# Kernel tuning notes

Measured on AMD Instinct MI355X. Metric: run time of the kernel, lower is better.

The kernel has to match this reference:

```python
import jax, jax.numpy as jnp
from jax import lax
import numpy as np

T, B, IN, H = 512, 256, 128, 512
TAU_MIN, TAU_MAX, DT = 0.2, 2.0, 0.1


def setup_inputs() -> dict:
    key = jax.random.key(0)
    ks = jax.random.split(key, 7)
    s_zh = 1.0 / np.sqrt(IN + H)  # torch Linear default init scale (fan_in)
    s_h = 1.0 / np.sqrt(H)
    return {
        "x_seq": jax.random.normal(ks[0], (T, B, IN), dtype=jnp.float32),
        "Wc": jax.random.uniform(ks[1], (IN + H, H), jnp.float32, -s_zh, s_zh),
        "bc": jax.random.uniform(ks[2], (H,), jnp.float32, -s_zh, s_zh),
        "Wt": jax.random.uniform(ks[3], (IN + H, H), jnp.float32, -s_zh, s_zh),
        "bt": jax.random.uniform(ks[4], (H,), jnp.float32, -s_zh, s_zh),
        "Wo": jax.random.uniform(ks[5], (H, 1), jnp.float32, -s_h, s_h),
        "bo": jax.random.uniform(ks[6], (1,), jnp.float32, -s_h, s_h),
    }


def reference(x_seq, Wc, bc, Wt, bt, Wo, bo):
    # Liquid time-constant RNN: sequential scan over T timesteps.
    def step(h, x_t):
        z = jnp.concatenate([x_t, h], axis=-1)           # [B, IN+H]
        candidate = jnp.tanh(z @ Wc + bc)                # [B, H]
        tau = TAU_MIN + jax.nn.sigmoid(z @ Wt + bt) * (TAU_MAX - TAU_MIN)
        h_next = h + DT * (-h + candidate) / tau         # ODE Euler update
        y_t = h_next @ Wo + bo                           # [B, 1]
        return h_next, (y_t, tau)

    h0 = jnp.zeros((x_seq.shape[1], Wc.shape[1]), dtype=x_seq.dtype)
    _, (y_seq, tau_seq) = lax.scan(step, h0, x_seq)
    return y_seq, tau_seq
```

## Files before the change

kernel.cpp:

```cpp
#include <hip/hip_runtime.h>
#include <stdint.h>

#define T_STEPS 512
#define BATCH   256
#define INP     128
#define HID     512
#define BGN     16
#define CGN     8
#define RB      16
#define CB      64
#define ZP      648

typedef float f32x4 __attribute__((ext_vector_type(4)));
typedef short s16x8 __attribute__((ext_vector_type(8)));
typedef unsigned short u16;
typedef unsigned int   u32;
typedef unsigned long long u64;

__device__ __forceinline__ u32 f2bf(float f) {
  union { float f; u32 u; } v; v.f = f;
  return (v.u + 0x7fffu + ((v.u >> 16) & 1u)) >> 16;
}


__global__ __launch_bounds__(256, 1)
void liquid_persistent(const float* __restrict__ x_seq,
                       const float* __restrict__ Wc, const float* __restrict__ bc,
                       const float* __restrict__ Wt, const float* __restrict__ bt,
                       const float* __restrict__ Wo, const float* __restrict__ bo,
                       float* __restrict__ y_out, float* __restrict__ tau_out,
                       u16* __restrict__ hb, int* __restrict__ flags)
{
  const int tid  = threadIdx.x;
  const int l    = tid & 63;
  const int w    = tid >> 6;
  const int quad = l >> 4;
  const int ln   = l & 15;
  const int bg   = blockIdx.x & (BGN - 1);
  const int cg   = blockIdx.x >> 4;
  const int R0   = bg * RB;
  const int C0   = cg * CB;
  const int cn   = C0 + w * 16 + ln;

  __shared__ u16 zS[RB][ZP];

  s16x8 wfC[20], wfT[20];
#pragma unroll
  for (int kt = 0; kt < 20; ++kt) {
#pragma unroll
    for (int j = 0; j < 8; ++j) {
      int k = kt * 32 + quad * 8 + j;
      wfC[kt][j] = (short)f2bf(Wc[k * HID + cn]);
      wfT[kt][j] = (short)f2bf(Wt[k * HID + cn]);
    }
  }

  const float bcv = bc[cn], btv = bt[cn], wov = Wo[cn];
  const float boadd = (cg == 0 && w == 0) ? bo[0] : 0.0f;
  float hm[4] = {0.f, 0.f, 0.f, 0.f};

  const int xrow = tid >> 4;
  const int xseg = tid & 15;
  int* myflags = flags + bg * (CGN * 16);

  {
    const float* xp = x_seq + ((size_t)0 * BATCH + R0 + xrow) * INP + xseg * 8;
    float4 a = *(const float4*)xp;
    float4 b = *(const float4*)(xp + 4);
    u64 w0 = (u64)f2bf(a.x) | ((u64)f2bf(a.y) << 16) |
             ((u64)f2bf(a.z) << 32) | ((u64)f2bf(a.w) << 48);
    u64 w1 = (u64)f2bf(b.x) | ((u64)f2bf(b.y) << 16) |
             ((u64)f2bf(b.z) << 32) | ((u64)f2bf(b.w) << 48);
    *(u64*)&zS[xrow][xseg * 8]     = w0;
    *(u64*)&zS[xrow][xseg * 8 + 4] = w1;
  }
  __syncthreads();

  for (int t = 0; t < T_STEPS; ++t) {
    const int p = t & 1;

    f32x4 aC0 = {0.f,0.f,0.f,0.f}, aC1 = {0.f,0.f,0.f,0.f};
    f32x4 aT0 = {0.f,0.f,0.f,0.f}, aT1 = {0.f,0.f,0.f,0.f};
    const u16* zb = &zS[ln][quad * 8];
    {
      s16x8 a0 = *(const s16x8*)(zb);
      s16x8 a1 = *(const s16x8*)(zb + 32);
      s16x8 a2 = *(const s16x8*)(zb + 64);
      s16x8 a3 = *(const s16x8*)(zb + 96);
      aC0 = __builtin_amdgcn_mfma_f32_16x16x32_bf16(a0, wfC[0], aC0, 0,0,0);
      aT0 = __builtin_amdgcn_mfma_f32_16x16x32_bf16(a0, wfT[0], aT0, 0,0,0);
      aC1 = __builtin_amdgcn_mfma_f32_16x16x32_bf16(a1, wfC[1], aC1, 0,0,0);
      aT1 = __builtin_amdgcn_mfma_f32_16x16x32_bf16(a1, wfT[1], aT1, 0,0,0);
      aC0 = __builtin_amdgcn_mfma_f32_16x16x32_bf16(a2, wfC[2], aC0, 0,0,0);
      aT0 = __builtin_amdgcn_mfma_f32_16x16x32_bf16(a2, wfT[2], aT0, 0,0,0);
      aC1 = __builtin_amdgcn_mfma_f32_16x16x32_bf16(a3, wfC[3], aC1, 0,0,0);
      aT1 = __builtin_amdgcn_mfma_f32_16x16x32_bf16(a3, wfT[3], aT1, 0,0,0);
    }

    const int tn = (t + 1 < T_STEPS) ? t + 1 : t;
    const float* xp = x_seq + ((size_t)tn * BATCH + R0 + xrow) * INP + xseg * 8;
    float4 xr0 = *(const float4*)xp;
    float4 xr1 = *(const float4*)(xp + 4);

    if (t > 0 && tid < CGN) {
      while (__hip_atomic_load(&myflags[tid * 16], __ATOMIC_RELAXED,
                               __HIP_MEMORY_SCOPE_AGENT) < t) { }
    }
    __syncthreads();

    {
      u64 hv[8];
      u64* hrow = (u64*)hb + ((size_t)p * BATCH + R0 + xrow) * (HID / 4);
#pragma unroll
      for (int i = 0; i < 8; ++i)
        hv[i] = __hip_atomic_load(&hrow[i * 16 + xseg], __ATOMIC_RELAXED,
                                  __HIP_MEMORY_SCOPE_AGENT);
#pragma unroll
      for (int i = 0; i < 8; ++i)
        *(u64*)&zS[xrow][INP + (i * 16 + xseg) * 4] = hv[i];
    }
    __syncthreads();

#pragma unroll
    for (int kt = 4; kt < 20; kt += 2) {
      s16x8 a0 = *(const s16x8*)(zb + kt * 32);
      s16x8 a1 = *(const s16x8*)(zb + kt * 32 + 32);
      aC0 = __builtin_amdgcn_mfma_f32_16x16x32_bf16(a0, wfC[kt],   aC0, 0,0,0);
      aT0 = __builtin_amdgcn_mfma_f32_16x16x32_bf16(a0, wfT[kt],   aT0, 0,0,0);
      aC1 = __builtin_amdgcn_mfma_f32_16x16x32_bf16(a1, wfC[kt+1], aC1, 0,0,0);
      aT1 = __builtin_amdgcn_mfma_f32_16x16x32_bf16(a1, wfT[kt+1], aT1, 0,0,0);
    }
    aC0 += aC1;
    aT0 += aT1;

    {
      u64 w0 = (u64)f2bf(xr0.x) | ((u64)f2bf(xr0.y) << 16) |
               ((u64)f2bf(xr0.z) << 32) | ((u64)f2bf(xr0.w) << 48);
      u64 w1 = (u64)f2bf(xr1.x) | ((u64)f2bf(xr1.y) << 16) |
               ((u64)f2bf(xr1.z) << 32) | ((u64)f2bf(xr1.w) << 48);
      *(u64*)&zS[xrow][xseg * 8]     = w0;
      *(u64*)&zS[xrow][xseg * 8 + 4] = w1;
    }

    float tauv[4];
#pragma unroll
    for (int r = 0; r < 4; ++r) {
      float pc = aC0[r] + bcv;
      float pt = aT0[r] + btv;
      pc = fminf(fmaxf(pc, -20.f), 20.f);
      float e  = __expf(2.f * pc);
      float cand = (e - 1.f) / (e + 1.f);
      float tau  = 0.2f + 1.8f / (1.f + __expf(-pt));
      hm[r] += 0.1f * (cand - hm[r]) / tau;
      tauv[r] = tau;
    }
#pragma unroll
    for (int r = 0; r < 4; ++r) {
      tau_out[((size_t)t * BATCH + R0 + quad * 4 + r) * HID + cn] = tauv[r];
    }

#pragma unroll
    for (int r = 0; r < 4; ++r) {
      u32 bits = f2bf(hm[r]);
      u32 ob   = (u32)__shfl_xor((int)bits, 1);
      if (!(ln & 1)) {
        u32 pk = bits | (ob << 16);
        u32* hp = (u32*)hb +
            (((size_t)(p ^ 1) * BATCH + R0 + quad * 4 + r) * HID + cn) / 2;
        __hip_atomic_store(hp, pk, __ATOMIC_RELAXED, __HIP_MEMORY_SCOPE_AGENT);
      }
    }

#pragma unroll
    for (int r = 0; r < 4; ++r) {
      float py = hm[r] * wov;
      py += __shfl_down(py, 8, 16);
      py += __shfl_down(py, 4, 16);
      py += __shfl_down(py, 2, 16);
      py += __shfl_down(py, 1, 16);
      if (ln == 0)
        atomicAdd(&y_out[t * BATCH + R0 + quad * 4 + r], py + boadd);
    }

    __syncthreads();
    if (tid == 0) {
      __hip_atomic_store(&myflags[cg * 16], t + 1, __ATOMIC_RELAXED,
                         __HIP_MEMORY_SCOPE_AGENT);
    }
  }
}

extern "C" void kernel_launch(void* const* d_in, const int* in_sizes, int n_in,
                              void* d_out, int out_size, void* d_ws, size_t ws_size,
                              hipStream_t stream) {
  (void)in_sizes; (void)n_in; (void)out_size; (void)ws_size;
  const float* x_seq = (const float*)d_in[0];
  const float* Wc    = (const float*)d_in[1];
  const float* bc    = (const float*)d_in[2];
  const float* Wt    = (const float*)d_in[3];
  const float* bt    = (const float*)d_in[4];
  const float* Wo    = (const float*)d_in[5];
  const float* bo    = (const float*)d_in[6];

  float* y_out   = (float*)d_out;
  float* tau_out = (float*)d_out + (size_t)T_STEPS * BATCH;

  const size_t HB_BYTES   = (size_t)2 * BATCH * HID * sizeof(u16);
  const size_t FLAG_BYTES = (size_t)BGN * CGN * 16 * sizeof(int);
  u16* hb    = (u16*)d_ws;
  int* flags = (int*)((char*)d_ws + HB_BYTES);

  hipMemsetAsync(d_out, 0, (size_t)T_STEPS * BATCH * sizeof(float), stream);
  hipMemsetAsync(d_ws, 0, HB_BYTES + FLAG_BYTES, stream);

  liquid_persistent<<<dim3(BGN * CGN), dim3(256), 0, stream>>>(
      x_seq, Wc, bc, Wt, bt, Wo, bo, y_out, tau_out, hb, flags);
}
```

Baseline: 2.033 ms.

## Replace flag barrier with sentinel-tagged 4-slot hidden-state ring buffer

Removes the per-step flag spin plus block barrier and instead encodes readiness in the data itself: a 4-deep ring of bf16 hidden-state buffers is poisoned with 0xFFFF sentinels, and each block polls only the seven peer column chunks until valid values appear. The block's own chunk is written straight from registers into shared memory, and the hidden-state publish is packed into 64-bit stores. This is meant to cut the latency of the inter-block handoff on the recurrent critical path, at the cost of relying on NaN-pattern sentinels never matching real bf16 data and extra store traffic for re-poisoning slots.

```diff
diff --git a/kernel.cpp b/kernel.cpp
--- a/kernel.cpp
+++ b/kernel.cpp
@@ -29,7 +29,7 @@
                        const float* __restrict__ Wt, const float* __restrict__ bt,
                        const float* __restrict__ Wo, const float* __restrict__ bo,
                        float* __restrict__ y_out, float* __restrict__ tau_out,
-                       u16* __restrict__ hb, int* __restrict__ flags)
+                       u16* __restrict__ hb)
 {
   const int tid  = threadIdx.x;
   const int l    = tid & 63;
@@ -61,7 +61,14 @@
 
   const int xrow = tid >> 4;
   const int xseg = tid & 15;
-  int* myflags = flags + bg * (CGN * 16);
+
+  int ii[7];
+#pragma unroll
+  for (int jx = 0; jx < 7; ++jx) ii[jx] = jx + (jx >= cg ? 1 : 0);
+
+  const size_t rowq = HID / 4;
+  u64* hbase = (u64*)(void*)hb;
+  const size_t myrow = (size_t)(R0 + xrow) * rowq;
 
   {
     const float* xp = x_seq + ((size_t)0 * BATCH + R0 + xrow) * INP + xseg * 8;
@@ -77,7 +84,15 @@
   __syncthreads();
 
   for (int t = 0; t < T_STEPS; ++t) {
-    const int p = t & 1;
+    const u64* rbase = hbase + (size_t)(t & 3) * BATCH * rowq + myrow + xseg;
+
+    u64 tmp[7];
+    if (t > 0) {
+#pragma unroll
+      for (int jx = 0; jx < 7; ++jx)
+        tmp[jx] = __hip_atomic_load(rbase + ii[jx] * 16, __ATOMIC_RELAXED,
+                                    __HIP_MEMORY_SCOPE_AGENT);
+    }
 
     f32x4 aC0 = {0.f,0.f,0.f,0.f}, aC1 = {0.f,0.f,0.f,0.f};
     f32x4 aT0 = {0.f,0.f,0.f,0.f}, aT1 = {0.f,0.f,0.f,0.f};
@@ -97,28 +112,58 @@
       aT1 = __builtin_amdgcn_mfma_f32_16x16x32_bf16(a3, wfT[3], aT1, 0,0,0);
     }
 
+    u64 hv[7];
+    if (t == 0) {
+#pragma unroll
+      for (int jx = 0; jx < 7; ++jx) hv[jx] = 0;
+    } else {
+      bool need[7];
+      int pending = 0;
+#pragma unroll
+      for (int jx = 0; jx < 7; ++jx) {
+        u64 v = tmp[jx];
+        bool ok = ((u32)v != 0xFFFFFFFFu) && ((u32)(v >> 32) != 0xFFFFFFFFu);
+        hv[jx] = v;
+        need[jx] = !ok;
+        pending += ok ? 0 : 1;
+      }
+      while (pending) {
+#pragma unroll
+        for (int jx = 0; jx < 7; ++jx)
+          if (need[jx])
+            tmp[jx] = __hip_atomic_load(rbase + ii[jx] * 16, __ATOMIC_RELAXED,
+                                        __HIP_MEMORY_SCOPE_AGENT);
+#pragma unroll
+        for (int jx = 0; jx < 7; ++jx)
+          if (need[jx]) {
+            u64 v = tmp[jx];
+            if (((u32)v != 0xFFFFFFFFu) && ((u32)(v >> 32) != 0xFFFFFFFFu)) {
+              hv[jx] = v;
+              need[jx] = false;
+              --pending;
+            }
+          }
+      }
+    }
+
+    {
+      u64* pp = hbase + (size_t)((t + 2) & 3) * BATCH * rowq + myrow
+              + (C0 / 4 + xseg);
+      __hip_atomic_store(pp, ~0ull, __ATOMIC_RELAXED, __HIP_MEMORY_SCOPE_AGENT);
+    }
+
     const int tn = (t + 1 < T_STEPS) ? t + 1 : t;
     const float* xp = x_seq + ((size_t)tn * BATCH + R0 + xrow) * INP + xseg * 8;
     float4 xr0 = *(const float4*)xp;
     float4 xr1 = *(const float4*)(xp + 4);
 
-    if (t > 0 && tid < CGN) {
-      while (__hip_atomic_load(&myflags[tid * 16], __ATOMIC_RELAXED,
-                               __HIP_MEMORY_SCOPE_AGENT) < t) { }
-    }
-    __syncthreads();
-
-    {
-      u64 hv[8];
-      u64* hrow = (u64*)hb + ((size_t)p * BATCH + R0 + xrow) * (HID / 4);
-#pragma unroll
-      for (int i = 0; i < 8; ++i)
-        hv[i] = __hip_atomic_load(&hrow[i * 16 + xseg], __ATOMIC_RELAXED,
-                                  __HIP_MEMORY_SCOPE_AGENT);
-#pragma unroll
-      for (int i = 0; i < 8; ++i)
-        *(u64*)&zS[xrow][INP + (i * 16 + xseg) * 4] = hv[i];
-    }
+#pragma unroll
+    for (int jx = 0; jx < 7; ++jx)
+      *(u64*)&zS[xrow][INP + (ii[jx] * 16 + xseg) * 4] = hv[jx];
+#pragma unroll
+    for (int r = 0; r < 4; ++r)
+      zS[quad * 4 + r][INP + cn] = (u16)f2bf(hm[r]);
+
     __syncthreads();
 
 #pragma unroll
@@ -154,23 +199,28 @@
       hm[r] += 0.1f * (cand - hm[r]) / tau;
       tauv[r] = tau;
     }
-#pragma unroll
-    for (int r = 0; r < 4; ++r) {
-      tau_out[((size_t)t * BATCH + R0 + quad * 4 + r) * HID + cn] = tauv[r];
-    }
+
+    asm volatile("s_waitcnt vmcnt(0)" ::: "memory");
 
 #pragma unroll
     for (int r = 0; r < 4; ++r) {
       u32 bits = f2bf(hm[r]);
-      u32 ob   = (u32)__shfl_xor((int)bits, 1);
-      if (!(ln & 1)) {
-        u32 pk = bits | (ob << 16);
-        u32* hp = (u32*)hb +
-            (((size_t)(p ^ 1) * BATCH + R0 + quad * 4 + r) * HID + cn) / 2;
-        __hip_atomic_store(hp, pk, __ATOMIC_RELAXED, __HIP_MEMORY_SCOPE_AGENT);
+      u32 b0   = bits | ((u32)__shfl_xor((int)bits, 1) << 16);
+      u64 q    = (u64)b0 | ((u64)(u32)__shfl_xor((int)b0, 2) << 32);
+      if (!(ln & 3)) {
+        u64* hp = hbase + (size_t)((t + 1) & 3) * BATCH * rowq
+                + (size_t)(R0 + quad * 4 + r) * rowq + (cn / 4);
+        __hip_atomic_store(hp, q, __ATOMIC_RELAXED, __HIP_MEMORY_SCOPE_AGENT);
       }
     }
 
+    __syncthreads();
+
+#pragma unroll
+    for (int r = 0; r < 4; ++r)
+      __builtin_nontemporal_store(
+          tauv[r],
+          &tau_out[((size_t)t * BATCH + R0 + quad * 4 + r) * HID + cn]);
 #pragma unroll
     for (int r = 0; r < 4; ++r) {
       float py = hm[r] * wov;
@@ -180,12 +230,6 @@
       py += __shfl_down(py, 1, 16);
       if (ln == 0)
         atomicAdd(&y_out[t * BATCH + R0 + quad * 4 + r], py + boadd);
-    }
-
-    __syncthreads();
-    if (tid == 0) {
-      __hip_atomic_store(&myflags[cg * 16], t + 1, __ATOMIC_RELAXED,
-                         __HIP_MEMORY_SCOPE_AGENT);
     }
   }
 }
@@ -205,14 +249,12 @@
   float* y_out   = (float*)d_out;
   float* tau_out = (float*)d_out + (size_t)T_STEPS * BATCH;
 
-  const size_t HB_BYTES   = (size_t)2 * BATCH * HID * sizeof(u16);
-  const size_t FLAG_BYTES = (size_t)BGN * CGN * 16 * sizeof(int);
-  u16* hb    = (u16*)d_ws;
-  int* flags = (int*)((char*)d_ws + HB_BYTES);
+  const size_t HB_BYTES = (size_t)4 * BATCH * HID * sizeof(u16);
+  u16* hb = (u16*)d_ws;
 
   hipMemsetAsync(d_out, 0, (size_t)T_STEPS * BATCH * sizeof(float), stream);
-  hipMemsetAsync(d_ws, 0, HB_BYTES + FLAG_BYTES, stream);
+  hipMemsetAsync(d_ws, 0xFF, HB_BYTES, stream);
 
   liquid_persistent<<<dim3(BGN * CGN), dim3(256), 0, stream>>>(
-      x_seq, Wc, bc, Wt, bt, Wo, bo, y_out, tau_out, hb, flags);
+      x_seq, Wc, bc, Wt, bt, Wo, bo, y_out, tau_out, hb);
 }
```

New measurement: 2.071 ms. Within noise of the previous version (+1.9%).
